# Optimization experiments

Measured on AMD Instinct MI355X. Metric: run time of the kernel, lower is better.

## Reference

```python
import jax, jax.numpy as jnp
import numpy as np

NEG_BIG = -9e15
ALPHA = 0.2  # LeakyReLU negative slope


def setup_inputs() -> dict:
    key = jax.random.key(0)
    k1, k2, k3, k4 = jax.random.split(key, 4)
    N, F_in, F_out = 8192, 256, 64
    inp = jax.random.normal(k1, (N, F_in), dtype=jnp.float32)
    adj = jax.random.randint(k2, (N, N), 0, 2, dtype=jnp.int32)
    W = jax.random.normal(k3, (F_in, F_out), dtype=jnp.float32) * 0.05
    a = jax.random.normal(k4, (2 * F_out, 1), dtype=jnp.float32) * 0.05
    return {"input": inp, "adj": adj, "W": W, "a": a}


def reference(input, adj, W, a):
    # h = X W : [N, F_out]
    h = input @ W
    F_out = W.shape[1]
    # a_input[i,j] = concat(h_i, h_j); a_input @ a = h@a1 broadcast over j + h@a2 broadcast over i.
    a1 = a[:F_out, 0]   # [F_out]
    a2 = a[F_out:, 0]   # [F_out]
    s1 = h @ a1         # [N]
    s2 = h @ a2         # [N]
    e = jax.nn.leaky_relu(s1[:, None] + s2[None, :], negative_slope=ALPHA)  # [N, N]
    att = jnp.where(adj > 0, e, jnp.float32(NEG_BIG))
    att = jax.nn.softmax(att, axis=1)
    # dropout is identity in eval mode (training=False)
    h_prime = att @ h   # [N, F_out]
    return jax.nn.elu(h_prime)
```

## Files before the change

kernel.cpp:

```cpp
#include <hip/hip_runtime.h>
#include <hip/hip_bf16.h>

typedef __bf16 bf16_t;
typedef __attribute__((ext_vector_type(8))) __bf16 bf16x8;
typedef __attribute__((ext_vector_type(4))) __bf16 bf16x4;
typedef __attribute__((ext_vector_type(4))) float floatx4;
typedef __attribute__((ext_vector_type(4))) int intx4;
typedef __attribute__((ext_vector_type(4))) unsigned uintx4;

#define NN 8192
#define FIN 256
#define FOUT 64
#define GAT_ALPHA 0.2f
#define JSPLIT 4
#define JSEG (NN / JSPLIT)
#define PHASEJ 256
#define NPHASE (JSEG / PHASEJ)
#define NSTEPS (JSEG / 32)
#define ROWSTRIDE 268

__global__ __launch_bounds__(256) void gat_h_kernel(
    const float* __restrict__ input,
    const float* __restrict__ W,
    const float* __restrict__ a,
    bf16_t* __restrict__ hT,
    float* __restrict__ e1g, float* __restrict__ f1g,
    unsigned* __restrict__ ef2g)
{
    alignas(16) __shared__ bf16_t in_lds[32][264];
    alignas(16) __shared__ bf16_t wt_lds[64][264];
    __shared__ float h_lds[32][65];

    const int t  = threadIdx.x;
    const int i0 = blockIdx.x * 32;

    #pragma unroll
    for (int v = 0; v < 8; v++) {
        int u  = v * 256 + t;
        int i  = u >> 6;
        int k4 = (u & 63) * 4;
        floatx4 x = *(const floatx4*)(input + (size_t)(i0 + i) * FIN + k4);
        bf16x4 b;
        #pragma unroll
        for (int e = 0; e < 4; e++) b[e] = (bf16_t)x[e];
        *(bf16x4*)(&in_lds[i][k4]) = b;
    }
    #pragma unroll
    for (int v = 0; v < 16; v++) {
        int u  = v * 256 + t;
        int k  = u >> 4;
        int f4 = (u & 15) * 4;
        floatx4 wv = *(const floatx4*)(W + k * FOUT + f4);
        #pragma unroll
        for (int e = 0; e < 4; e++) wt_lds[f4 + e][k] = (bf16_t)wv[e];
    }
    __syncthreads();

    const int wave = t >> 6;
    const int lane = t & 63;
    const int i16  = (wave & 1) * 16;
    const int f32  = (wave >> 1) * 32;
    const int lm   = lane & 15;
    const int lq   = lane >> 4;

    floatx4 acc0 = {0.f, 0.f, 0.f, 0.f};
    floatx4 acc1 = {0.f, 0.f, 0.f, 0.f};
    #pragma unroll
    for (int ks = 0; ks < 8; ks++) {
        int ko = ks * 32 + lq * 8;
        bf16x8 af = *(const bf16x8*)(&in_lds[i16 + lm][ko]);
        bf16x8 b0 = *(const bf16x8*)(&wt_lds[f32 + lm][ko]);
        bf16x8 b1 = *(const bf16x8*)(&wt_lds[f32 + 16 + lm][ko]);
        acc0 = __builtin_amdgcn_mfma_f32_16x16x32_bf16(af, b0, acc0, 0, 0, 0);
        acc1 = __builtin_amdgcn_mfma_f32_16x16x32_bf16(af, b1, acc1, 0, 0, 0);
    }

    #pragma unroll
    for (int c = 0; c < 2; c++) {
        floatx4 acc = c ? acc1 : acc0;
        int f  = f32 + c * 16 + lm;
        int ib = i0 + i16 + lq * 4;
        bf16x4 hp;
        #pragma unroll
        for (int r = 0; r < 4; r++) hp[r] = (bf16_t)acc[r];
        *(bf16x4*)(hT + (size_t)f * NN + ib) = hp;
    }
    #pragma unroll
    for (int c = 0; c < 2; c++) {
        floatx4 acc = c ? acc1 : acc0;
        #pragma unroll
        for (int r = 0; r < 4; r++)
            h_lds[i16 + lq * 4 + r][f32 + c * 16 + lm] = acc[r];
    }
    __syncthreads();

    if (t < 64) {
        int r   = t & 31;
        int sel = t >> 5;
        const float* av = a + sel * FOUT;
        float s = 0.f;
        #pragma unroll 8
        for (int f = 0; f < FOUT; f++) s += h_lds[r][f] * av[f];
        int gi = i0 + r;
        float E = expf(s);
        float F = expf(GAT_ALPHA * s);
        if (sel == 0) {
            e1g[gi] = E; f1g[gi] = F;
        } else {
            unsigned eb = __builtin_bit_cast(unsigned short, (bf16_t)E);
            unsigned fb = __builtin_bit_cast(unsigned short, (bf16_t)F);
            ef2g[gi] = (fb << 16) | eb;
        }
    }
}

__global__ __launch_bounds__(192) void gat_att_kernel(
    const int* __restrict__ adj,
    const bf16_t* __restrict__ hT,
    const float* __restrict__ e1g, const float* __restrict__ f1g,
    const unsigned* __restrict__ ef2g,
    float* __restrict__ pacc,
    float* __restrict__ prs)
{
    __shared__ int abuf[2][32 * ROWSTRIDE];

    const int t    = threadIdx.x;
    const int wave = t >> 6;
    const int lane = t & 63;
    const int bx   = blockIdx.x;
    const int js   = blockIdx.y;
    const int jb   = js * JSEG;
    const int bi0  = bx * 32;

    if (wave == 2) {
        #pragma unroll
        for (int r = 0; r < 32; r++)
            __builtin_amdgcn_global_load_lds(
                (const __attribute__((address_space(1))) unsigned*)
                    (adj + (size_t)(bi0 + r) * NN + jb + lane * 4),
                (__attribute__((address_space(3))) unsigned*)
                    (&abuf[0][r * ROWSTRIDE]),
                16, 0, 0);
        for (int p = 0; p < NPHASE; p++) {
            asm volatile("s_waitcnt vmcnt(0)" ::: "memory");
            asm volatile("s_barrier" ::: "memory");
            if (p + 1 < NPHASE) {
                int* dst = abuf[(p + 1) & 1];
                #pragma unroll
                for (int r = 0; r < 32; r++)
                    __builtin_amdgcn_global_load_lds(
                        (const __attribute__((address_space(1))) unsigned*)
                            (adj + (size_t)(bi0 + r) * NN + jb
                             + (p + 1) * PHASEJ + lane * 4),
                        (__attribute__((address_space(3))) unsigned*)
                            (dst + r * ROWSTRIDE),
                        16, 0, 0);
            }
        }
        return;
    }

    const int m   = lane & 15;
    const int q   = lane >> 4;
    const int i0  = bi0 + wave * 16;
    const int lr  = wave * 16 + m;

    const float E1 = e1g[i0 + m];
    const float F1 = f1g[i0 + m];

    const unsigned* efp = ef2g + jb + q * 8;
    const bf16_t*   htp = hT + (size_t)m * NN + jb + q * 8;

    floatx4 acc[4];
    #pragma unroll
    for (int c = 0; c < 4; c++) acc[c] = (floatx4){0.f, 0.f, 0.f, 0.f};
    floatx4 acc4 = {0.f, 0.f, 0.f, 0.f};

    bf16x8 ones8;
    #pragma unroll
    for (int e = 0; e < 8; e++) ones8[e] = (bf16_t)1.0f;

    uintx4 e0 = *(const uintx4*)(efp);
    uintx4 e1 = *(const uintx4*)(efp + 4);
    bf16x8 hb[4];
    #pragma unroll
    for (int c = 0; c < 4; c++)
        hb[c] = *(const bf16x8*)(htp + (size_t)c * 16 * NN);

    for (int p = 0; p < NPHASE; p++) {
        asm volatile("s_barrier" ::: "memory");
        const int* ap = abuf[p & 1] + lr * ROWSTRIDE + q * 8;

        #pragma unroll
        for (int ks = 0; ks < 8; ks++) {
            intx4 a0 = *(const intx4*)(ap + ks * 32);
            intx4 a1 = *(const intx4*)(ap + ks * 32 + 4);

            uintx4 ce0 = e0, ce1 = e1;
            bf16x8 ch0 = hb[0], ch1 = hb[1], ch2 = hb[2], ch3 = hb[3];
            const int s = p * 8 + ks;
            if (s + 1 < NSTEPS) {
                e0 = *(const uintx4*)(efp + (s + 1) * 32);
                e1 = *(const uintx4*)(efp + (s + 1) * 32 + 4);
                #pragma unroll
                for (int c = 0; c < 4; c++)
                    hb[c] = *(const bf16x8*)(htp + (size_t)c * 16 * NN
                                             + (s + 1) * 32);
            }

            bf16x8 wf;
            #pragma unroll
            for (int e = 0; e < 8; e++) {
                int av     = (e < 4) ? a0[e] : a1[e - 4];
                unsigned v = (e < 4) ? ce0[e] : ce1[e - 4];
                float e2 = __builtin_bit_cast(float, v << 16);
                float f2 = __builtin_bit_cast(float, v & 0xffff0000u);
                float pv = fmaxf(E1 * e2, F1 * f2);
                wf[e] = (bf16_t)((av > 0) ? pv : 0.f);
            }
            acc[0] = __builtin_amdgcn_mfma_f32_16x16x32_bf16(wf, ch0, acc[0], 0, 0, 0);
            acc[1] = __builtin_amdgcn_mfma_f32_16x16x32_bf16(wf, ch1, acc[1], 0, 0, 0);
            acc[2] = __builtin_amdgcn_mfma_f32_16x16x32_bf16(wf, ch2, acc[2], 0, 0, 0);
            acc[3] = __builtin_amdgcn_mfma_f32_16x16x32_bf16(wf, ch3, acc[3], 0, 0, 0);
            acc4   = __builtin_amdgcn_mfma_f32_16x16x32_bf16(wf, ones8, acc4, 0, 0, 0);
        }
    }

    if (m == 0) {
        #pragma unroll
        for (int r = 0; r < 4; r++)
            prs[(size_t)js * NN + i0 + q * 4 + r] = acc4[r];
    }

    float* pa = pacc + (size_t)js * NN * FOUT;
    #pragma unroll
    for (int c = 0; c < 4; c++) {
        #pragma unroll
        for (int r = 0; r < 4; r++)
            pa[(size_t)(i0 + q * 4 + r) * FOUT + c * 16 + m] = acc[c][r];
    }
}

__global__ __launch_bounds__(256) void gat_combine_kernel(
    const float* __restrict__ pacc,
    const float* __restrict__ prs,
    float* __restrict__ out)
{
    int idx = blockIdx.x * 256 + threadIdx.x;
    int i   = idx >> 4;
    floatx4 s = {0.f, 0.f, 0.f, 0.f};
    float rs  = 0.f;
    #pragma unroll
    for (int js = 0; js < JSPLIT; js++) {
        s  += *(const floatx4*)(pacc + (size_t)js * NN * FOUT + (size_t)idx * 4);
        rs += prs[(size_t)js * NN + i];
    }
    float rinv = (rs > 0.f) ? 1.0f / rs : 0.f;
    floatx4 r;
    #pragma unroll
    for (int e = 0; e < 4; e++) {
        float x = s[e] * rinv;
        r[e] = (x > 0.f) ? x : (expf(x) - 1.0f);
    }
    *(floatx4*)(out + (size_t)idx * 4) = r;
}

extern "C" void kernel_launch(void* const* d_in, const int* in_sizes, int n_in,
                              void* d_out, int out_size, void* d_ws, size_t ws_size,
                              hipStream_t stream) {
    const float* input = (const float*)d_in[0];
    const int*   adj   = (const int*)d_in[1];
    const float* W     = (const float*)d_in[2];
    const float* a     = (const float*)d_in[3];
    float*       out   = (float*)d_out;

    char* ws = (char*)d_ws;
    bf16_t*   hT   = (bf16_t*)ws;
    float*    e1g  = (float*)(ws + (1 << 20));
    float*    f1g  = e1g + NN;
    unsigned* ef2g = (unsigned*)(f1g + NN);
    float*    pacc = (float*)(ef2g + NN);
    float*    prs  = pacc + (size_t)JSPLIT * NN * FOUT;

    gat_h_kernel<<<NN / 32, 256, 0, stream>>>(input, W, a, hT, e1g, f1g, ef2g);

    dim3 gridB(NN / 32, JSPLIT);
    gat_att_kernel<<<gridB, 192, 0, stream>>>(adj, hT, e1g, f1g, ef2g,
                                              pacc, prs);

    gat_combine_kernel<<<NN * FOUT / 4 / 256, 256, 0, stream>>>(pacc, prs, out);
}
```

Measured before the change: 434.0 us.

## Pack adjacency into bitmask in a separate kernel and drop LDS staging

```diff
diff --git a/kernel.cpp b/kernel.cpp
--- a/kernel.cpp
+++ b/kernel.cpp
@@ -14,10 +14,24 @@
 #define GAT_ALPHA 0.2f
 #define JSPLIT 4
 #define JSEG (NN / JSPLIT)
-#define PHASEJ 256
-#define NPHASE (JSEG / PHASEJ)
 #define NSTEPS (JSEG / 32)
-#define ROWSTRIDE 268
+#define NWORDS (NN / 32)
+
+__global__ __launch_bounds__(256) void adj_pack_kernel(
+    const int* __restrict__ adj, unsigned* __restrict__ mask)
+{
+    const size_t t = (size_t)blockIdx.x * 256 + threadIdx.x;
+    const int* p = adj + t * 32;
+    unsigned m = 0;
+    #pragma unroll
+    for (int g = 0; g < 8; g++) {
+        intx4 v = *(const intx4*)(p + g * 4);
+        #pragma unroll
+        for (int e = 0; e < 4; e++)
+            m |= (v[e] > 0) ? (1u << (g * 4 + e)) : 0u;
+    }
+    mask[t] = m;
+}
 
 __global__ __launch_bounds__(256) void gat_h_kernel(
     const float* __restrict__ input,
@@ -114,60 +128,28 @@
     }
 }
 
-__global__ __launch_bounds__(192) void gat_att_kernel(
-    const int* __restrict__ adj,
+__global__ __launch_bounds__(128, 2) void gat_att_kernel(
+    const unsigned* __restrict__ mask,
     const bf16_t* __restrict__ hT,
     const float* __restrict__ e1g, const float* __restrict__ f1g,
     const unsigned* __restrict__ ef2g,
     float* __restrict__ pacc,
     float* __restrict__ prs)
 {
-    __shared__ int abuf[2][32 * ROWSTRIDE];
-
     const int t    = threadIdx.x;
     const int wave = t >> 6;
     const int lane = t & 63;
-    const int bx   = blockIdx.x;
+    const int m    = lane & 15;
+    const int q    = lane >> 4;
+    const int i0   = blockIdx.x * 32 + wave * 16;
     const int js   = blockIdx.y;
     const int jb   = js * JSEG;
-    const int bi0  = bx * 32;
-
-    if (wave == 2) {
-        #pragma unroll
-        for (int r = 0; r < 32; r++)
-            __builtin_amdgcn_global_load_lds(
-                (const __attribute__((address_space(1))) unsigned*)
-                    (adj + (size_t)(bi0 + r) * NN + jb + lane * 4),
-                (__attribute__((address_space(3))) unsigned*)
-                    (&abuf[0][r * ROWSTRIDE]),
-                16, 0, 0);
-        for (int p = 0; p < NPHASE; p++) {
-            asm volatile("s_waitcnt vmcnt(0)" ::: "memory");
-            asm volatile("s_barrier" ::: "memory");
-            if (p + 1 < NPHASE) {
-                int* dst = abuf[(p + 1) & 1];
-                #pragma unroll
-                for (int r = 0; r < 32; r++)
-                    __builtin_amdgcn_global_load_lds(
-                        (const __attribute__((address_space(1))) unsigned*)
-                            (adj + (size_t)(bi0 + r) * NN + jb
-                             + (p + 1) * PHASEJ + lane * 4),
-                        (__attribute__((address_space(3))) unsigned*)
-                            (dst + r * ROWSTRIDE),
-                        16, 0, 0);
-            }
-        }
-        return;
-    }
-
-    const int m   = lane & 15;
-    const int q   = lane >> 4;
-    const int i0  = bi0 + wave * 16;
-    const int lr  = wave * 16 + m;
-
-    const float E1 = e1g[i0 + m];
-    const float F1 = f1g[i0 + m];
-
+    const int row  = i0 + m;
+
+    const float E1 = e1g[row];
+    const float F1 = f1g[row];
+
+    const unsigned* mp  = mask + (size_t)row * NWORDS + jb / 32;
     const unsigned* efp = ef2g + jb + q * 8;
     const bf16_t*   htp = hT + (size_t)m * NN + jb + q * 8;
 
@@ -180,6 +162,7 @@
     #pragma unroll
     for (int e = 0; e < 8; e++) ones8[e] = (bf16_t)1.0f;
 
+    uintx4 mw = *(const uintx4*)(mp);
     uintx4 e0 = *(const uintx4*)(efp);
     uintx4 e1 = *(const uintx4*)(efp + 4);
     bf16x8 hb[4];
@@ -187,18 +170,17 @@
     for (int c = 0; c < 4; c++)
         hb[c] = *(const bf16x8*)(htp + (size_t)c * 16 * NN);
 
-    for (int p = 0; p < NPHASE; p++) {
-        asm volatile("s_barrier" ::: "memory");
-        const int* ap = abuf[p & 1] + lr * ROWSTRIDE + q * 8;
-
-        #pragma unroll
-        for (int ks = 0; ks < 8; ks++) {
-            intx4 a0 = *(const intx4*)(ap + ks * 32);
-            intx4 a1 = *(const intx4*)(ap + ks * 32 + 4);
+    for (int g = 0; g < NSTEPS / 4; g++) {
+        uintx4 mc = mw;
+        if (g + 1 < NSTEPS / 4) mw = *(const uintx4*)(mp + (g + 1) * 4);
+
+        #pragma unroll
+        for (int ks = 0; ks < 4; ks++) {
+            const int s = g * 4 + ks;
+            const unsigned bits = (mc[ks] >> (q * 8)) & 0xFFu;
 
             uintx4 ce0 = e0, ce1 = e1;
             bf16x8 ch0 = hb[0], ch1 = hb[1], ch2 = hb[2], ch3 = hb[3];
-            const int s = p * 8 + ks;
             if (s + 1 < NSTEPS) {
                 e0 = *(const uintx4*)(efp + (s + 1) * 32);
                 e1 = *(const uintx4*)(efp + (s + 1) * 32 + 4);
@@ -211,12 +193,11 @@
             bf16x8 wf;
             #pragma unroll
             for (int e = 0; e < 8; e++) {
-                int av     = (e < 4) ? a0[e] : a1[e - 4];
                 unsigned v = (e < 4) ? ce0[e] : ce1[e - 4];
                 float e2 = __builtin_bit_cast(float, v << 16);
                 float f2 = __builtin_bit_cast(float, v & 0xffff0000u);
                 float pv = fmaxf(E1 * e2, F1 * f2);
-                wf[e] = (bf16_t)((av > 0) ? pv : 0.f);
+                wf[e] = (bf16_t)((bits & (1u << e)) ? pv : 0.f);
             }
             acc[0] = __builtin_amdgcn_mfma_f32_16x16x32_bf16(wf, ch0, acc[0], 0, 0, 0);
             acc[1] = __builtin_amdgcn_mfma_f32_16x16x32_bf16(wf, ch1, acc[1], 0, 0, 0);
@@ -279,13 +260,16 @@
     float*    e1g  = (float*)(ws + (1 << 20));
     float*    f1g  = e1g + NN;
     unsigned* ef2g = (unsigned*)(f1g + NN);
-    float*    pacc = (float*)(ef2g + NN);
+    unsigned* mask = ef2g + NN;
+    float*    pacc = (float*)(mask + (size_t)NN * NWORDS);
     float*    prs  = pacc + (size_t)JSPLIT * NN * FOUT;
 
+    adj_pack_kernel<<<(NN / 32) * (NN / 256), 256, 0, stream>>>(adj, mask);
+
     gat_h_kernel<<<NN / 32, 256, 0, stream>>>(input, W, a, hT, e1g, f1g, ef2g);
 
     dim3 gridB(NN / 32, JSPLIT);
-    gat_att_kernel<<<gridB, 192, 0, stream>>>(adj, hT, e1g, f1g, ef2g,
+    gat_att_kernel<<<gridB, 128, 0, stream>>>(mask, hT, e1g, f1g, ef2g,
                                               pacc, prs);
 
     gat_combine_kernel<<<NN * FOUT / 4 / 256, 256, 0, stream>>>(pacc, prs, out);
```

Result: slower. 442.8 us (+2.0%).
